# Performance work log

Hardware: AMD Instinct MI355X
Metric: run time of the kernel (lower is better)

Reference implementation:

```python
import jax, jax.numpy as jnp
import numpy as np

EPS = 1e-8  # matches init eps


def setup_inputs() -> dict:
    key = jax.random.key(0)
    ks = jax.random.split(key, 6)
    B, LA, LB, Dh, P = 2, 512, 512, 1024, 64
    return {
        "h_a": jax.random.normal(ks[0], (B, LA, Dh), dtype=jnp.float32),
        "h_b": jax.random.normal(ks[1], (B, LB, Dh), dtype=jnp.float32),
        "Wa": jax.random.normal(ks[2], (Dh, P), dtype=jnp.float32) * 0.02,
        "ba": jax.random.normal(ks[3], (P,), dtype=jnp.float32) * 0.02,
        "Wb": jax.random.normal(ks[4], (Dh, P), dtype=jnp.float32) * 0.02,
        "bb": jax.random.normal(ks[5], (P,), dtype=jnp.float32) * 0.02,
    }


def reference(h_a, h_b, Wa, ba, Wb, bb):
    # Project + exact GELU (torch default)
    z_a = jax.nn.gelu(h_a @ Wa + ba, approximate=False)  # [B,LA,P]
    z_b = jax.nn.gelu(h_b @ Wb + bb, approximate=False)  # [B,LB,P]
    B, LA, P = z_a.shape
    LB = z_b.shape[1]
    # Channel-first broadcasts: [B,P,LA,LB]
    za = jnp.transpose(z_a, (0, 2, 1))[:, :, :, None]  # [B,P,LA,1]
    zb = jnp.transpose(z_b, (0, 2, 1))[:, :, None, :]  # [B,P,1,LB]
    za_e = jnp.broadcast_to(za, (B, P, LA, LB))
    zb_e = jnp.broadcast_to(zb, (B, P, LA, LB))
    diff = jnp.abs(za_e - zb_e)
    prod = za_e * zb_e
    # cosine similarity channel, computed from per-residue stats (no D-expanded tensor)
    dot = jnp.einsum("bip,bjp->bij", z_a, z_b)[:, None]  # [B,1,LA,LB]
    na = jnp.sqrt(jnp.sum(z_a * z_a, axis=-1) + EPS)  # [B,LA]
    nb = jnp.sqrt(jnp.sum(z_b * z_b, axis=-1) + EPS)  # [B,LB]
    sim = dot / (na[:, None, :, None] * nb[:, None, None, :])
    # channel order matches torch cat([z_a, z_b, diff, prod, sim], -1).permute(0,3,1,2)
    return jnp.concatenate([za_e, zb_e, diff, prod, sim], axis=1)  # [B,4P+1,LA,LB]
```

## Files before the change

kernel.cpp:

```cpp
#include <hip/hip_runtime.h>
#include <math.h>

#define B_    2
#define LA_   512
#define LB_   512
#define DH_   1024
#define P_    64
#define NCH_  257
#define EPS_  1e-8f
#define CH_   ((size_t)LA_ * LB_)
#define TILES_ 4
#define TROWS_ (LA_ / TILES_)

__global__ __launch_bounds__(256) void proj_gelu_kernel(
    const float* __restrict__ h_a, const float* __restrict__ Wa,
    const float* __restrict__ ba,
    const float* __restrict__ h_b, const float* __restrict__ Wb,
    const float* __restrict__ bb,
    float* __restrict__ zat,
    float* __restrict__ zbt,
    float* __restrict__ rna,
    float* __restrict__ rnb)
{
    __shared__ __align__(16) float hs[DH_];
    __shared__ __align__(16) float partial[256 * 4];

    const int side = blockIdx.x >> 10;
    const int row  = blockIdx.x & 1023;
    const int b    = row >> 9;
    const int i    = row & 511;
    const int tid  = threadIdx.x;

    const float* h    = side ? h_b : h_a;
    const float* W    = side ? Wb  : Wa;
    const float* bias = side ? bb  : ba;
    float* z  = side ? zbt : zat;
    float* rn = side ? rnb : rna;

    ((float4*)hs)[tid] = ((const float4*)(h + (size_t)row * DH_))[tid];
    __syncthreads();

    const int pg = (tid & 15) * 4;
    const int q  = tid >> 4;
    const float* Wq = W + (size_t)(q * 64) * P_ + pg;
    float4 acc = make_float4(0.f, 0.f, 0.f, 0.f);
    #pragma unroll 8
    for (int k = 0; k < 64; ++k) {
        const float  hv = hs[q * 64 + k];
        const float4 w  = *(const float4*)(Wq + (size_t)k * P_);
        acc.x = fmaf(hv, w.x, acc.x);
        acc.y = fmaf(hv, w.y, acc.y);
        acc.z = fmaf(hv, w.z, acc.z);
        acc.w = fmaf(hv, w.w, acc.w);
    }
    *(float4*)(partial + tid * 4) = acc;
    __syncthreads();

    if (tid < 64) {
        float v = partial[tid];
        #pragma unroll
        for (int qq = 1; qq < 16; ++qq)
            v += partial[qq * 64 + tid];
        v += bias[tid];
        float g = 0.5f * v * (1.f + erff(v * 0.70710678118654752f));

        z[((size_t)(b * P_ + tid)) * 512 + i] = g;

        float s = g * g;
        #pragma unroll
        for (int off = 32; off > 0; off >>= 1)
            s += __shfl_down(s, off, 64);
        if (tid == 0)
            rn[row] = 1.f / sqrtf(s + EPS_);
    }
}

__global__ __launch_bounds__(256) void map_kernel(
    const float* __restrict__ zat,
    const float* __restrict__ zbt,
    const float* __restrict__ rna,
    const float* __restrict__ rnb,
    float* __restrict__ out)
{
    __shared__ __align__(16) float smem[P_ * 16];

    const int b   = blockIdx.z;
    const int tid = threadIdx.x;

    if (blockIdx.x < 256) {
        float* zbrow = smem;
        float* zacol = smem + LB_;

        const int ch  = blockIdx.x;
        const int t   = ch >> 6;
        const int p   = ch & 63;
        const int i0  = blockIdx.y * TROWS_;

        if (tid < 128)
            ((float4*)zbrow)[tid] = ((const float4*)(zbt + (size_t)(b * P_ + p) * 512))[tid];
        else if (tid < 160)
            ((float4*)zacol)[tid - 128] =
                ((const float4*)(zat + (size_t)(b * P_ + p) * 512 + i0))[tid - 128];
        __syncthreads();

        const int half = tid >> 7;
        const int jj   = (tid & 127) * 4;
        const float4 zbv = *(const float4*)(zbrow + jj);

        float* op = out + (size_t)(b * NCH_ + ch) * CH_ + (size_t)(i0 + half) * LB_ + jj;

        if (t == 0) {
            #pragma unroll 4
            for (int it = 0; it < TROWS_ / 2; ++it) {
                const float a = zacol[2 * it + half];
                *(float4*)op = make_float4(a, a, a, a);
                op += 2 * LB_;
            }
        } else if (t == 1) {
            #pragma unroll 4
            for (int it = 0; it < TROWS_ / 2; ++it) {
                *(float4*)op = make_float4(zbv.x, zbv.y, zbv.z, zbv.w);
                op += 2 * LB_;
            }
        } else if (t == 2) {
            #pragma unroll 4
            for (int it = 0; it < TROWS_ / 2; ++it) {
                const float a = zacol[2 * it + half];
                *(float4*)op = make_float4(fabsf(a - zbv.x), fabsf(a - zbv.y),
                                           fabsf(a - zbv.z), fabsf(a - zbv.w));
                op += 2 * LB_;
            }
        } else {
            #pragma unroll 4
            for (int it = 0; it < TROWS_ / 2; ++it) {
                const float a = zacol[2 * it + half];
                *(float4*)op = make_float4(a * zbv.x, a * zbv.y, a * zbv.z, a * zbv.w);
                op += 2 * LB_;
            }
        }
    } else {
        const int s  = blockIdx.x - 256;
        const int i0 = s * 16;
        const int j0 = blockIdx.y * 128;
        float* zas = smem;

        {
            const int p  = tid >> 2;
            const int i4 = (tid & 3) * 4;
            *(float4*)(zas + p * 16 + i4) =
                *(const float4*)(zat + (size_t)(b * P_ + p) * 512 + i0 + i4);
        }
        __syncthreads();

        const int r = tid >> 7;
        const int j = j0 + (tid & 127);

        float acc[8];
        #pragma unroll
        for (int u = 0; u < 8; ++u) acc[u] = 0.f;

        for (int p = 0; p < P_; ++p) {
            const float zb = zbt[(size_t)(b * P_ + p) * 512 + j];
            #pragma unroll
            for (int u = 0; u < 8; ++u)
                acc[u] = fmaf(zas[p * 16 + r * 8 + u], zb, acc[u]);
        }

        const float rbj = rnb[b * 512 + j];
        float* plane = out + (size_t)(b * NCH_ + 256) * CH_;
        #pragma unroll
        for (int u = 0; u < 8; ++u) {
            const int i = i0 + r * 8 + u;
            plane[(size_t)i * LB_ + j] = acc[u] * rna[b * 512 + i] * rbj;
        }
    }
}

extern "C" void kernel_launch(void* const* d_in, const int* in_sizes, int n_in,
                              void* d_out, int out_size, void* d_ws, size_t ws_size,
                              hipStream_t stream)
{
    const float* h_a = (const float*)d_in[0];
    const float* h_b = (const float*)d_in[1];
    const float* Wa  = (const float*)d_in[2];
    const float* ba  = (const float*)d_in[3];
    const float* Wb  = (const float*)d_in[4];
    const float* bb  = (const float*)d_in[5];
    float* out = (float*)d_out;

    float* ws  = (float*)d_ws;
    float* zat = ws;
    float* zbt = zat + (size_t)B_ * P_ * LA_;
    float* rna = zbt + (size_t)B_ * P_ * LB_;
    float* rnb = rna + (size_t)B_ * LA_;

    proj_gelu_kernel<<<2 * B_ * LA_, 256, 0, stream>>>(
        h_a, Wa, ba, h_b, Wb, bb, zat, zbt, rna, rnb);
    map_kernel<<<dim3(256 + LA_ / 16, TILES_, B_), 256, 0, stream>>>(
        zat, zbt, rna, rnb, out);
}
```

Before: 556.1 us.

## Flatten broadcast-map writes into grid-stride loop and put similarity blocks first

Replaces the per-channel tiled write blocks with a 1D grid-stride loop over all float4 output elements. Each thread computes its plane, channel type and position from a flat index and loads z values straight from global memory instead of staging them in shared memory. The similarity (dot-product) blocks now take the first block indices, so they are scheduled ahead of the streaming writers. This aims at better load balance and store throughput for the write-bound map, at the cost of more index arithmetic and redundant global or cache loads per element.

New measurement: 545.9 us, median of 2. About the same (-1.8%).

```diff
diff --git a/kernel.cpp b/kernel.cpp
--- a/kernel.cpp
+++ b/kernel.cpp
@@ -9,8 +9,11 @@
 #define NCH_  257
 #define EPS_  1e-8f
 #define CH_   ((size_t)LA_ * LB_)
-#define TILES_ 4
-#define TROWS_ (LA_ / TILES_)
+
+#define SIMBLK_  256
+#define WBLK_    1792
+#define NQ_      ((size_t)512 * CH_ / 4)
+#define WSTRIDE_ ((size_t)WBLK_ * 256)
 
 __global__ __launch_bounds__(256) void proj_gelu_kernel(
     const float* __restrict__ h_a, const float* __restrict__ Wa,
@@ -82,67 +85,46 @@
     const float* __restrict__ rnb,
     float* __restrict__ out)
 {
-    __shared__ __align__(16) float smem[P_ * 16];
+    const int tid = threadIdx.x;
+    const int bid = blockIdx.x;
 
-    const int b   = blockIdx.z;
-    const int tid = threadIdx.x;
+    if (bid >= SIMBLK_) {
+        const int wid = bid - SIMBLK_;
+        size_t q = (size_t)wid * 256 + tid;
+        #pragma unroll 2
+        for (; q < NQ_; q += WSTRIDE_) {
+            const int plane = (int)(q >> 16);
+            const int b     = plane >> 8;
+            const int ch    = plane & 255;
+            const int t     = ch >> 6;
+            const int p     = ch & 63;
+            const int w4    = (int)(q & 65535);
+            const int i     = w4 >> 7;
+            const int j     = (w4 & 127) << 2;
 
-    if (blockIdx.x < 256) {
-        float* zbrow = smem;
-        float* zacol = smem + LB_;
+            const size_t zoff = ((size_t)((b << 6) + p)) << 9;
+            const float  a    = zat[zoff + i];
+            const float4 zb   = *(const float4*)(zbt + zoff + j);
 
-        const int ch  = blockIdx.x;
-        const int t   = ch >> 6;
-        const int p   = ch & 63;
-        const int i0  = blockIdx.y * TROWS_;
+            float4 v;
+            if (t == 0)       v = make_float4(a, a, a, a);
+            else if (t == 1)  v = zb;
+            else if (t == 2)  v = make_float4(fabsf(a - zb.x), fabsf(a - zb.y),
+                                              fabsf(a - zb.z), fabsf(a - zb.w));
+            else              v = make_float4(a * zb.x, a * zb.y,
+                                              a * zb.z, a * zb.w);
 
-        if (tid < 128)
-            ((float4*)zbrow)[tid] = ((const float4*)(zbt + (size_t)(b * P_ + p) * 512))[tid];
-        else if (tid < 160)
-            ((float4*)zacol)[tid - 128] =
-                ((const float4*)(zat + (size_t)(b * P_ + p) * 512 + i0))[tid - 128];
-        __syncthreads();
-
-        const int half = tid >> 7;
-        const int jj   = (tid & 127) * 4;
-        const float4 zbv = *(const float4*)(zbrow + jj);
-
-        float* op = out + (size_t)(b * NCH_ + ch) * CH_ + (size_t)(i0 + half) * LB_ + jj;
-
-        if (t == 0) {
-            #pragma unroll 4
-            for (int it = 0; it < TROWS_ / 2; ++it) {
-                const float a = zacol[2 * it + half];
-                *(float4*)op = make_float4(a, a, a, a);
-                op += 2 * LB_;
-            }
-        } else if (t == 1) {
-            #pragma unroll 4
-            for (int it = 0; it < TROWS_ / 2; ++it) {
-                *(float4*)op = make_float4(zbv.x, zbv.y, zbv.z, zbv.w);
-                op += 2 * LB_;
-            }
-        } else if (t == 2) {
-            #pragma unroll 4
-            for (int it = 0; it < TROWS_ / 2; ++it) {
-                const float a = zacol[2 * it + half];
-                *(float4*)op = make_float4(fabsf(a - zbv.x), fabsf(a - zbv.y),
-                                           fabsf(a - zbv.z), fabsf(a - zbv.w));
-                op += 2 * LB_;
-            }
-        } else {
-            #pragma unroll 4
-            for (int it = 0; it < TROWS_ / 2; ++it) {
-                const float a = zacol[2 * it + half];
-                *(float4*)op = make_float4(a * zbv.x, a * zbv.y, a * zbv.z, a * zbv.w);
-                op += 2 * LB_;
-            }
+            float* op = out + (((size_t)(b * NCH_ + ch)) << 18) + ((size_t)w4 << 2);
+            *(float4*)op = v;
         }
     } else {
-        const int s  = blockIdx.x - 256;
-        const int i0 = s * 16;
-        const int j0 = blockIdx.y * 128;
-        float* zas = smem;
+        __shared__ __align__(16) float zas[P_ * 16];
+
+        const int s  = bid;
+        const int b  = s >> 7;
+        const int r  = s & 127;
+        const int i0 = (r >> 2) * 16;
+        const int j0 = (r & 3) * 128;
 
         {
             const int p  = tid >> 2;
@@ -152,8 +134,8 @@
         }
         __syncthreads();
 
-        const int r = tid >> 7;
-        const int j = j0 + (tid & 127);
+        const int rr = tid >> 7;
+        const int j  = j0 + (tid & 127);
 
         float acc[8];
         #pragma unroll
@@ -163,14 +145,14 @@
             const float zb = zbt[(size_t)(b * P_ + p) * 512 + j];
             #pragma unroll
             for (int u = 0; u < 8; ++u)
-                acc[u] = fmaf(zas[p * 16 + r * 8 + u], zb, acc[u]);
+                acc[u] = fmaf(zas[p * 16 + rr * 8 + u], zb, acc[u]);
         }
 
         const float rbj = rnb[b * 512 + j];
         float* plane = out + (size_t)(b * NCH_ + 256) * CH_;
         #pragma unroll
         for (int u = 0; u < 8; ++u) {
-            const int i = i0 + r * 8 + u;
+            const int i = i0 + rr * 8 + u;
             plane[(size_t)i * LB_ + j] = acc[u] * rna[b * 512 + i] * rbj;
         }
     }
@@ -196,6 +178,6 @@
 
     proj_gelu_kernel<<<2 * B_ * LA_, 256, 0, stream>>>(
         h_a, Wa, ba, h_b, Wb, bb, zat, zbt, rna, rnb);
-    map_kernel<<<dim3(256 + LA_ / 16, TILES_, B_), 256, 0, stream>>>(
+    map_kernel<<<dim3(SIMBLK_ + WBLK_), 256, 0, stream>>>(
         zat, zbt, rna, rnb, out);
 }
```
